# Optimization experiments

Hardware: AMD Instinct MI355X
Metric: run time of the kernel (lower is better)

## Reference

```python
import jax, jax.numpy as jnp
import numpy as np

B = 65536
IN = 64
H = 128
OUT = 2


def setup_inputs() -> dict:
    key = jax.random.key(0)
    ks = jax.random.split(key, 16)
    s_in = 1.0 / np.sqrt(IN)
    s_h = 1.0 / np.sqrt(H)
    d = {}
    d["x"] = jax.random.normal(ks[0], (B, IN), dtype=jnp.float32)
    # initial state (module resets to zeros per day)
    d["h0"] = jnp.zeros((H,), dtype=jnp.float32)
    d["c0"] = jnp.zeros((B, H), dtype=jnp.float32)
    # input->hidden linears (with bias), torch Linear layout [out, in]
    for i, name in enumerate(["f", "i", "o", "c"]):
        d[f"Wx{name}"] = jax.random.uniform(ks[1 + i], (H, IN), jnp.float32, -s_in, s_in)
        d[f"bx{name}"] = jax.random.uniform(ks[5 + i], (H,), jnp.float32, -s_in, s_in)
        d[f"Wh{name}"] = jax.random.uniform(ks[9 + i], (H, H), jnp.float32, -s_h, s_h)
    d["Wy"] = jax.random.uniform(ks[13], (OUT, H), jnp.float32, -s_h, s_h)
    d["by"] = jax.random.uniform(ks[14], (OUT,), jnp.float32, -s_h, s_h)
    return d


def reference(x, h0, c0, Wxf, bxf, Wxi, bxi, Wxo, bxo, Wxc, bxc, Whf, Whi, Who, Whc, Wy, by):
    # hidden recurrent contributions (h0 is a length-H vector, broadcast over batch)
    hi = h0 @ Whi.T  # [H]
    hf = h0 @ Whf.T
    ho = h0 @ Who.T
    hc = h0 @ Whc.T
    i = jax.nn.sigmoid(x @ Wxi.T + bxi + hi)  # [B, H]
    f = jax.nn.sigmoid(x @ Wxf.T + bxf + hf)
    o = jax.nn.sigmoid(x @ Wxo.T + bxo + ho)
    c_til = jnp.tanh(x @ Wxc.T + bxc + hc)
    c = f * c0 + i * c_til
    h = o * jnp.tanh(c)
    y_hat = h @ Wy.T + by  # [B, OUT]
    return y_hat
```

## Files before the change

kernel.cpp:

```cpp
#include <hip/hip_runtime.h>


#define B_SIZE 65536

typedef __bf16 bf16x8 __attribute__((ext_vector_type(8)));
typedef __bf16 bf16x4 __attribute__((ext_vector_type(4)));
typedef float f32x4 __attribute__((ext_vector_type(4)));

__device__ __forceinline__ float fsig(float x) {
    float e = __builtin_amdgcn_exp2f(-1.442695040888963f * x);
    return __builtin_amdgcn_rcpf(1.0f + e);
}
__device__ __forceinline__ float ftanh(float x) {
    float e = __builtin_amdgcn_exp2f(2.885390081777927f * x);
    return 1.0f - 2.0f * __builtin_amdgcn_rcpf(e + 1.0f);
}

__global__ void bias_kernel(const float* __restrict__ h0,
                            const float* __restrict__ Whf, const float* __restrict__ Whi,
                            const float* __restrict__ Who, const float* __restrict__ Whc,
                            const float* __restrict__ bxf, const float* __restrict__ bxi,
                            const float* __restrict__ bxo, const float* __restrict__ bxc,
                            float* __restrict__ bias512) {
    int j = blockIdx.x * 64 + threadIdx.x;
    int g = j >> 7, r = j & 127;
    const float* Wh = (g == 0) ? Whf : (g == 1) ? Whi : (g == 2) ? Who : Whc;
    const float* bx = (g == 0) ? bxf : (g == 1) ? bxi : (g == 2) ? bxo : bxc;
    float s = bx[r];
    const float4* row = (const float4*)(Wh + r * 128);
    const float4* h4  = (const float4*)h0;
#pragma unroll 8
    for (int k = 0; k < 32; ++k) {
        float4 a = row[k], b = h4[k];
        s += a.x * b.x + a.y * b.y + a.z * b.z + a.w * b.w;
    }
    bias512[j] = s;
}

__global__ void prep_kernel(const float* __restrict__ Wxf, const float* __restrict__ Wxi,
                            const float* __restrict__ Wxo, const float* __restrict__ Wxc,
                            __bf16* __restrict__ frags) {
    int t = blockIdx.x * 64 + threadIdx.x;
    int w    = t >> 10;
    int g    = (t >> 8) & 3;
    int cb   = (t >> 7) & 1;
    int kb   = (t >> 6) & 1;
    int lane = t & 63;
    const float* Wx = (g == 0) ? Wxf : (g == 1) ? Wxi : (g == 2) ? Wxo : Wxc;
    const int n = w * 32 + cb * 16 + (lane & 15);
    const float* p = Wx + n * 64 + kb * 32 + (lane >> 4) * 8;
    float4 lo = *(const float4*)p;
    float4 hi = *(const float4*)(p + 4);
    bf16x8 v;
    v[0] = (__bf16)lo.x; v[1] = (__bf16)lo.y; v[2] = (__bf16)lo.z; v[3] = (__bf16)lo.w;
    v[4] = (__bf16)hi.x; v[5] = (__bf16)hi.y; v[6] = (__bf16)hi.z; v[7] = (__bf16)hi.w;
    *(bf16x8*)(frags + (size_t)t * 8) = v;
}

__launch_bounds__(256, 2)
__global__ void lstm_kernel(const float* __restrict__ x, const float* __restrict__ c0,
                            const __bf16* __restrict__ frags,
                            const float* __restrict__ Wy, const float* __restrict__ by,
                            const float* __restrict__ bias512, float* __restrict__ out) {
    __shared__ __bf16 xs[2][1024];
    __shared__ float cs[2][16 * 132];
    __shared__ float yred[4][128][2];

    const int tid  = threadIdx.x;
    const int lane = tid & 63;
    const int w    = tid >> 6;
    const int q    = lane >> 4;
    const int n15  = lane & 15;

    bf16x8 bw[4][2][2];
    float biasv[4][2];
#pragma unroll
    for (int g = 0; g < 4; ++g)
#pragma unroll
        for (int cb = 0; cb < 2; ++cb) {
            biasv[g][cb] = bias512[g * 128 + w * 32 + cb * 16 + n15];
#pragma unroll
            for (int kb = 0; kb < 2; ++kb)
                bw[g][cb][kb] = *(const bf16x8*)(frags +
                    (size_t)(((w * 16 + g * 4 + cb * 2 + kb) * 64 + lane)) * 8);
        }
    float wyv[2][2];
#pragma unroll
    for (int o = 0; o < 2; ++o)
#pragma unroll
        for (int cb = 0; cb < 2; ++cb)
            wyv[o][cb] = Wy[o * 128 + w * 32 + cb * 16 + n15];
    const float by0 = by[0], by1 = by[1];

    constexpr int ITERS = (B_SIZE / 16) / 512;
    const int tile0 = blockIdx.x * ITERS;

    const int xrow = tid >> 4;
    const int k4   = (tid & 15) * 4;
    const int sidx = (k4 >> 5) * 512 + ((k4 & 31) >> 3) * 128 + xrow * 8 + (k4 & 7);

    const int ccol = (tid & 15) * 8;
    const int cidx = xrow * 132 + ccol;

    float4 xr  = *(const float4*)(x  + (size_t)(tile0 * 16 + xrow) * 64 + k4);
    float4 cpa = *(const float4*)(c0 + (size_t)(tile0 * 16 + xrow) * 128 + ccol);
    float4 cpb = *(const float4*)(c0 + (size_t)(tile0 * 16 + xrow) * 128 + ccol + 4);
    {
        bf16x4 v; v[0] = (__bf16)xr.x; v[1] = (__bf16)xr.y; v[2] = (__bf16)xr.z; v[3] = (__bf16)xr.w;
        *(bf16x4*)&xs[0][sidx] = v;
        *(float4*)&cs[0][cidx] = cpa;
        *(float4*)&cs[0][cidx + 4] = cpb;
    }
    xr  = *(const float4*)(x  + (size_t)((tile0 + 1) * 16 + xrow) * 64 + k4);
    cpa = *(const float4*)(c0 + (size_t)((tile0 + 1) * 16 + xrow) * 128 + ccol);
    cpb = *(const float4*)(c0 + (size_t)((tile0 + 1) * 16 + xrow) * 128 + ccol + 4);
    __syncthreads();

#pragma unroll
    for (int it = 0; it < ITERS; ++it) {
        const int cur = it & 1;

        bf16x8 a0 = *(const bf16x8*)&xs[cur][lane * 8];
        bf16x8 a1 = *(const bf16x8*)&xs[cur][512 + lane * 8];

        float c0v[2][4];
#pragma unroll
        for (int cb = 0; cb < 2; ++cb)
#pragma unroll
            for (int r = 0; r < 4; ++r)
                c0v[cb][r] = cs[cur][(q * 4 + r) * 132 + w * 32 + cb * 16 + n15];

        if (it + 1 < ITERS) {
            bf16x4 v; v[0] = (__bf16)xr.x; v[1] = (__bf16)xr.y; v[2] = (__bf16)xr.z; v[3] = (__bf16)xr.w;
            *(bf16x4*)&xs[cur ^ 1][sidx] = v;
            *(float4*)&cs[cur ^ 1][cidx] = cpa;
            *(float4*)&cs[cur ^ 1][cidx + 4] = cpb;
            if (it + 2 < ITERS) {
                const int tn = tile0 + it + 2;
                xr  = *(const float4*)(x  + (size_t)(tn * 16 + xrow) * 64 + k4);
                cpa = *(const float4*)(c0 + (size_t)(tn * 16 + xrow) * 128 + ccol);
                cpb = *(const float4*)(c0 + (size_t)(tn * 16 + xrow) * 128 + ccol + 4);
            }
        }

        f32x4 acc[4][2];
#pragma unroll
        for (int g = 0; g < 4; ++g)
#pragma unroll
            for (int cb = 0; cb < 2; ++cb) {
                float b = biasv[g][cb];
                f32x4 t = {b, b, b, b};
                acc[g][cb] = t;
            }
#pragma unroll
        for (int g = 0; g < 4; ++g)
#pragma unroll
            for (int cb = 0; cb < 2; ++cb) {
                acc[g][cb] = __builtin_amdgcn_mfma_f32_16x16x32_bf16(a0, bw[g][cb][0], acc[g][cb], 0, 0, 0);
                acc[g][cb] = __builtin_amdgcn_mfma_f32_16x16x32_bf16(a1, bw[g][cb][1], acc[g][cb], 0, 0, 0);
            }

        float p0[4] = {0.f, 0.f, 0.f, 0.f};
        float p1[4] = {0.f, 0.f, 0.f, 0.f};
#pragma unroll
        for (int cb = 0; cb < 2; ++cb)
#pragma unroll
            for (int r = 0; r < 4; ++r) {
                float fg = fsig(acc[0][cb][r]);
                float ig = fsig(acc[1][cb][r]);
                float og = fsig(acc[2][cb][r]);
                float ct = ftanh(acc[3][cb][r]);
                float c  = fg * c0v[cb][r] + ig * ct;
                float h  = og * ftanh(c);
                p0[r] += h * wyv[0][cb];
                p1[r] += h * wyv[1][cb];
            }
#pragma unroll
        for (int m = 1; m < 16; m <<= 1) {
#pragma unroll
            for (int r = 0; r < 4; ++r) {
                p0[r] += __shfl_xor(p0[r], m, 64);
                p1[r] += __shfl_xor(p1[r], m, 64);
            }
        }
        if (n15 == 0) {
#pragma unroll
            for (int r = 0; r < 4; ++r) {
                yred[w][it * 16 + q * 4 + r][0] = p0[r];
                yred[w][it * 16 + q * 4 + r][1] = p1[r];
            }
        }
        __syncthreads();
    }

    if (tid < 128) {
        float s0 = by0 + yred[0][tid][0] + yred[1][tid][0] + yred[2][tid][0] + yred[3][tid][0];
        float s1 = by1 + yred[0][tid][1] + yred[1][tid][1] + yred[2][tid][1] + yred[3][tid][1];
        float2 s = {s0, s1};
        *(float2*)(out + (size_t)(tile0 * 16 + tid) * 2) = s;
    }
}

extern "C" void kernel_launch(void* const* d_in, const int* in_sizes, int n_in,
                              void* d_out, int out_size, void* d_ws, size_t ws_size,
                              hipStream_t stream) {
    const float* x   = (const float*)d_in[0];
    const float* h0  = (const float*)d_in[1];
    const float* c0  = (const float*)d_in[2];
    const float* Wxf = (const float*)d_in[3];
    const float* bxf = (const float*)d_in[4];
    const float* Whf = (const float*)d_in[5];
    const float* Wxi = (const float*)d_in[6];
    const float* bxi = (const float*)d_in[7];
    const float* Whi = (const float*)d_in[8];
    const float* Wxo = (const float*)d_in[9];
    const float* bxo = (const float*)d_in[10];
    const float* Who = (const float*)d_in[11];
    const float* Wxc = (const float*)d_in[12];
    const float* bxc = (const float*)d_in[13];
    const float* Whc = (const float*)d_in[14];
    const float* Wy  = (const float*)d_in[15];
    const float* by  = (const float*)d_in[16];
    float* out = (float*)d_out;
    float* bias512 = (float*)d_ws;
    __bf16* frags  = (__bf16*)((float*)d_ws + 512);

    bias_kernel<<<8, 64, 0, stream>>>(h0, Whf, Whi, Who, Whc, bxf, bxi, bxo, bxc, bias512);
    prep_kernel<<<64, 64, 0, stream>>>(Wxf, Wxi, Wxo, Wxc, frags);
    lstm_kernel<<<512, 256, 0, stream>>>(x, c0, frags, Wy, by, bias512, out);
}
```

Baseline: 126.1 us.

## Merge prep kernels and double LSTM block size to 32 rows per tile

Folds the bias and weight-fragment prep kernels into one launch to cut a kernel launch. The LSTM kernel now uses 512 threads (8 waves), with two row-halves of 4 waves each processing 32 batch rows per iteration. That halves the iteration count and the number of per-iteration barriers relative to rows processed. It also raises LDS usage and the register pressure allowed under the larger launch bounds.

```diff
diff --git a/kernel.cpp b/kernel.cpp
--- a/kernel.cpp
+++ b/kernel.cpp
@@ -16,59 +16,61 @@
     return 1.0f - 2.0f * __builtin_amdgcn_rcpf(e + 1.0f);
 }
 
-__global__ void bias_kernel(const float* __restrict__ h0,
+__global__ void prep_kernel(const float* __restrict__ h0,
                             const float* __restrict__ Whf, const float* __restrict__ Whi,
                             const float* __restrict__ Who, const float* __restrict__ Whc,
                             const float* __restrict__ bxf, const float* __restrict__ bxi,
                             const float* __restrict__ bxo, const float* __restrict__ bxc,
-                            float* __restrict__ bias512) {
-    int j = blockIdx.x * 64 + threadIdx.x;
-    int g = j >> 7, r = j & 127;
-    const float* Wh = (g == 0) ? Whf : (g == 1) ? Whi : (g == 2) ? Who : Whc;
-    const float* bx = (g == 0) ? bxf : (g == 1) ? bxi : (g == 2) ? bxo : bxc;
-    float s = bx[r];
-    const float4* row = (const float4*)(Wh + r * 128);
-    const float4* h4  = (const float4*)h0;
+                            const float* __restrict__ Wxf, const float* __restrict__ Wxi,
+                            const float* __restrict__ Wxo, const float* __restrict__ Wxc,
+                            float* __restrict__ bias512, __bf16* __restrict__ frags) {
+    if (blockIdx.x < 8) {
+        int j = blockIdx.x * 64 + threadIdx.x;
+        int g = j >> 7, r = j & 127;
+        const float* Wh = (g == 0) ? Whf : (g == 1) ? Whi : (g == 2) ? Who : Whc;
+        const float* bx = (g == 0) ? bxf : (g == 1) ? bxi : (g == 2) ? bxo : bxc;
+        float s = bx[r];
+        const float4* row = (const float4*)(Wh + r * 128);
+        const float4* h4  = (const float4*)h0;
 #pragma unroll 8
-    for (int k = 0; k < 32; ++k) {
-        float4 a = row[k], b = h4[k];
-        s += a.x * b.x + a.y * b.y + a.z * b.z + a.w * b.w;
-    }
-    bias512[j] = s;
-}
-
-__global__ void prep_kernel(const float* __restrict__ Wxf, const float* __restrict__ Wxi,
-                            const float* __restrict__ Wxo, const float* __restrict__ Wxc,
-                            __bf16* __restrict__ frags) {
-    int t = blockIdx.x * 64 + threadIdx.x;
-    int w    = t >> 10;
-    int g    = (t >> 8) & 3;
-    int cb   = (t >> 7) & 1;
-    int kb   = (t >> 6) & 1;
-    int lane = t & 63;
-    const float* Wx = (g == 0) ? Wxf : (g == 1) ? Wxi : (g == 2) ? Wxo : Wxc;
-    const int n = w * 32 + cb * 16 + (lane & 15);
-    const float* p = Wx + n * 64 + kb * 32 + (lane >> 4) * 8;
-    float4 lo = *(const float4*)p;
-    float4 hi = *(const float4*)(p + 4);
-    bf16x8 v;
-    v[0] = (__bf16)lo.x; v[1] = (__bf16)lo.y; v[2] = (__bf16)lo.z; v[3] = (__bf16)lo.w;
-    v[4] = (__bf16)hi.x; v[5] = (__bf16)hi.y; v[6] = (__bf16)hi.z; v[7] = (__bf16)hi.w;
-    *(bf16x8*)(frags + (size_t)t * 8) = v;
-}
-
-__launch_bounds__(256, 2)
+        for (int k = 0; k < 32; ++k) {
+            float4 a = row[k], b = h4[k];
+            s += a.x * b.x + a.y * b.y + a.z * b.z + a.w * b.w;
+        }
+        bias512[j] = s;
+    } else {
+        int t = (blockIdx.x - 8) * 64 + threadIdx.x;
+        int w    = t >> 10;
+        int g    = (t >> 8) & 3;
+        int cb   = (t >> 7) & 1;
+        int kb   = (t >> 6) & 1;
+        int lane = t & 63;
+        const float* Wx = (g == 0) ? Wxf : (g == 1) ? Wxi : (g == 2) ? Wxo : Wxc;
+        const int n = w * 32 + cb * 16 + (lane & 15);
+        const float* p = Wx + n * 64 + kb * 32 + (lane >> 4) * 8;
+        float4 lo = *(const float4*)p;
+        float4 hi = *(const float4*)(p + 4);
+        bf16x8 v;
+        v[0] = (__bf16)lo.x; v[1] = (__bf16)lo.y; v[2] = (__bf16)lo.z; v[3] = (__bf16)lo.w;
+        v[4] = (__bf16)hi.x; v[5] = (__bf16)hi.y; v[6] = (__bf16)hi.z; v[7] = (__bf16)hi.w;
+        *(bf16x8*)(frags + (size_t)t * 8) = v;
+    }
+}
+
+__launch_bounds__(512, 2)
 __global__ void lstm_kernel(const float* __restrict__ x, const float* __restrict__ c0,
                             const __bf16* __restrict__ frags,
                             const float* __restrict__ Wy, const float* __restrict__ by,
                             const float* __restrict__ bias512, float* __restrict__ out) {
-    __shared__ __bf16 xs[2][1024];
-    __shared__ float cs[2][16 * 132];
+    __shared__ __bf16 xs[2][2][1024];
+    __shared__ float cs[2][32 * 132];
     __shared__ float yred[4][128][2];
 
     const int tid  = threadIdx.x;
     const int lane = tid & 63;
     const int w    = tid >> 6;
+    const int rh   = w >> 2;
+    const int wc   = w & 3;
     const int q    = lane >> 4;
     const int n15  = lane & 15;
 
@@ -78,68 +80,69 @@
     for (int g = 0; g < 4; ++g)
 #pragma unroll
         for (int cb = 0; cb < 2; ++cb) {
-            biasv[g][cb] = bias512[g * 128 + w * 32 + cb * 16 + n15];
+            biasv[g][cb] = bias512[g * 128 + wc * 32 + cb * 16 + n15];
 #pragma unroll
             for (int kb = 0; kb < 2; ++kb)
                 bw[g][cb][kb] = *(const bf16x8*)(frags +
-                    (size_t)(((w * 16 + g * 4 + cb * 2 + kb) * 64 + lane)) * 8);
+                    (size_t)(((wc * 16 + g * 4 + cb * 2 + kb) * 64 + lane)) * 8);
         }
     float wyv[2][2];
 #pragma unroll
     for (int o = 0; o < 2; ++o)
 #pragma unroll
         for (int cb = 0; cb < 2; ++cb)
-            wyv[o][cb] = Wy[o * 128 + w * 32 + cb * 16 + n15];
+            wyv[o][cb] = Wy[o * 128 + wc * 32 + cb * 16 + n15];
     const float by0 = by[0], by1 = by[1];
 
-    constexpr int ITERS = (B_SIZE / 16) / 512;
-    const int tile0 = blockIdx.x * ITERS;
+    constexpr int ITERS = (B_SIZE / 32) / 512;
+    const int row0 = blockIdx.x * (ITERS * 32);
 
     const int xrow = tid >> 4;
     const int k4   = (tid & 15) * 4;
-    const int sidx = (k4 >> 5) * 512 + ((k4 & 31) >> 3) * 128 + xrow * 8 + (k4 & 7);
+    const int rhs  = xrow >> 4;
+    const int sidx = (k4 >> 5) * 512 + ((k4 & 31) >> 3) * 128 + (xrow & 15) * 8 + (k4 & 7);
 
     const int ccol = (tid & 15) * 8;
     const int cidx = xrow * 132 + ccol;
 
-    float4 xr  = *(const float4*)(x  + (size_t)(tile0 * 16 + xrow) * 64 + k4);
-    float4 cpa = *(const float4*)(c0 + (size_t)(tile0 * 16 + xrow) * 128 + ccol);
-    float4 cpb = *(const float4*)(c0 + (size_t)(tile0 * 16 + xrow) * 128 + ccol + 4);
+    float4 xr  = *(const float4*)(x  + (size_t)(row0 + xrow) * 64 + k4);
+    float4 cpa = *(const float4*)(c0 + (size_t)(row0 + xrow) * 128 + ccol);
+    float4 cpb = *(const float4*)(c0 + (size_t)(row0 + xrow) * 128 + ccol + 4);
     {
         bf16x4 v; v[0] = (__bf16)xr.x; v[1] = (__bf16)xr.y; v[2] = (__bf16)xr.z; v[3] = (__bf16)xr.w;
-        *(bf16x4*)&xs[0][sidx] = v;
+        *(bf16x4*)&xs[0][rhs][sidx] = v;
         *(float4*)&cs[0][cidx] = cpa;
         *(float4*)&cs[0][cidx + 4] = cpb;
     }
-    xr  = *(const float4*)(x  + (size_t)((tile0 + 1) * 16 + xrow) * 64 + k4);
-    cpa = *(const float4*)(c0 + (size_t)((tile0 + 1) * 16 + xrow) * 128 + ccol);
-    cpb = *(const float4*)(c0 + (size_t)((tile0 + 1) * 16 + xrow) * 128 + ccol + 4);
+    xr  = *(const float4*)(x  + (size_t)(row0 + 32 + xrow) * 64 + k4);
+    cpa = *(const float4*)(c0 + (size_t)(row0 + 32 + xrow) * 128 + ccol);
+    cpb = *(const float4*)(c0 + (size_t)(row0 + 32 + xrow) * 128 + ccol + 4);
     __syncthreads();
 
 #pragma unroll
     for (int it = 0; it < ITERS; ++it) {
         const int cur = it & 1;
 
-        bf16x8 a0 = *(const bf16x8*)&xs[cur][lane * 8];
-        bf16x8 a1 = *(const bf16x8*)&xs[cur][512 + lane * 8];
+        bf16x8 a0 = *(const bf16x8*)&xs[cur][rh][lane * 8];
+        bf16x8 a1 = *(const bf16x8*)&xs[cur][rh][512 + lane * 8];
 
         float c0v[2][4];
 #pragma unroll
         for (int cb = 0; cb < 2; ++cb)
 #pragma unroll
             for (int r = 0; r < 4; ++r)
-                c0v[cb][r] = cs[cur][(q * 4 + r) * 132 + w * 32 + cb * 16 + n15];
+                c0v[cb][r] = cs[cur][(rh * 16 + q * 4 + r) * 132 + wc * 32 + cb * 16 + n15];
 
         if (it + 1 < ITERS) {
             bf16x4 v; v[0] = (__bf16)xr.x; v[1] = (__bf16)xr.y; v[2] = (__bf16)xr.z; v[3] = (__bf16)xr.w;
-            *(bf16x4*)&xs[cur ^ 1][sidx] = v;
+            *(bf16x4*)&xs[cur ^ 1][rhs][sidx] = v;
             *(float4*)&cs[cur ^ 1][cidx] = cpa;
             *(float4*)&cs[cur ^ 1][cidx + 4] = cpb;
             if (it + 2 < ITERS) {
-                const int tn = tile0 + it + 2;
-                xr  = *(const float4*)(x  + (size_t)(tn * 16 + xrow) * 64 + k4);
-                cpa = *(const float4*)(c0 + (size_t)(tn * 16 + xrow) * 128 + ccol);
-                cpb = *(const float4*)(c0 + (size_t)(tn * 16 + xrow) * 128 + ccol + 4);
+                const int rn = row0 + (it + 2) * 32;
+                xr  = *(const float4*)(x  + (size_t)(rn + xrow) * 64 + k4);
+                cpa = *(const float4*)(c0 + (size_t)(rn + xrow) * 128 + ccol);
+                cpb = *(const float4*)(c0 + (size_t)(rn + xrow) * 128 + ccol + 4);
             }
         }
 
@@ -186,8 +189,8 @@
         if (n15 == 0) {
 #pragma unroll
             for (int r = 0; r < 4; ++r) {
-                yred[w][it * 16 + q * 4 + r][0] = p0[r];
-                yred[w][it * 16 + q * 4 + r][1] = p1[r];
+                yred[wc][it * 32 + rh * 16 + q * 4 + r][0] = p0[r];
+                yred[wc][it * 32 + rh * 16 + q * 4 + r][1] = p1[r];
             }
         }
         __syncthreads();
@@ -197,7 +200,7 @@
         float s0 = by0 + yred[0][tid][0] + yred[1][tid][0] + yred[2][tid][0] + yred[3][tid][0];
         float s1 = by1 + yred[0][tid][1] + yred[1][tid][1] + yred[2][tid][1] + yred[3][tid][1];
         float2 s = {s0, s1};
-        *(float2*)(out + (size_t)(tile0 * 16 + tid) * 2) = s;
+        *(float2*)(out + (size_t)(row0 + tid) * 2) = s;
     }
 }
 
@@ -225,7 +228,7 @@
     float* bias512 = (float*)d_ws;
     __bf16* frags  = (__bf16*)((float*)d_ws + 512);
 
-    bias_kernel<<<8, 64, 0, stream>>>(h0, Whf, Whi, Who, Whc, bxf, bxi, bxo, bxc, bias512);
-    prep_kernel<<<64, 64, 0, stream>>>(Wxf, Wxi, Wxo, Wxc, frags);
-    lstm_kernel<<<512, 256, 0, stream>>>(x, c0, frags, Wy, by, bias512, out);
-}
+    prep_kernel<<<72, 64, 0, stream>>>(h0, Whf, Whi, Who, Whc, bxf, bxi, bxo, bxc,
+                                       Wxf, Wxi, Wxo, Wxc, bias512, frags);
+    lstm_kernel<<<512, 512, 0, stream>>>(x, c0, frags, Wy, by, bias512, out);
+}
```

After: 127.0 us (median of 2 runs). About the same (+0.7%).
